# Kernel tuning notes

Measured on AMD Instinct MI355X. Metric: run time of the kernel, lower is better.

Reference implementation:

```python
import jax, jax.numpy as jnp
import numpy as np

B, S, D = 32, 1024, 1024
H = 16            # attention heads
T = 8             # num_tasks (probe tokens)
E = 8             # num_experts
K = 2             # top_k
HID = 4 * D       # expert hidden dim
EPS = 1e-5


def setup_inputs() -> dict:
    key = jax.random.key(0)
    ks = jax.random.split(key, 12)
    sd = 1.0 / np.sqrt(D)
    inp = {
        "x": jax.random.normal(ks[0], (B, S, D), jnp.float32),
        "probe": jax.random.normal(ks[1], (1, T, D), jnp.float32) * 0.02,
        "in_proj_w": jax.random.normal(ks[2], (3 * D, D), jnp.float32) * sd,
        "in_proj_b": jnp.zeros((3 * D,), jnp.float32),
        "out_proj_w": jax.random.normal(ks[3], (D, D), jnp.float32) * sd,
        "out_proj_b": jnp.zeros((D,), jnp.float32),
        "ln_gamma": jnp.ones((D,), jnp.float32),
        "ln_beta": jnp.zeros((D,), jnp.float32),
        "gate_w": jax.random.normal(ks[4], (T, D, E), jnp.float32) * sd,  # per-task gate (task-aware)
        "w1": jax.random.normal(ks[5], (E, D, HID), jnp.float32) * sd,
        "b1": jnp.zeros((E, HID), jnp.float32),
        "w2": jax.random.normal(ks[6], (E, HID, D), jnp.float32) / np.sqrt(HID),
        "b2": jnp.zeros((E, D), jnp.float32),
    }
    return inp


def reference(x, probe, in_proj_w, in_proj_b, out_proj_w, out_proj_b,
              ln_gamma, ln_beta, gate_w, w1, b1, w2, b2):
    b, s, d = x.shape
    t = probe.shape[1]
    dh = d // H
    # --- multihead cross attention: query = probe, key/value = x ---
    wq, wk, wv = in_proj_w[:d], in_proj_w[d:2 * d], in_proj_w[2 * d:]
    bq, bk, bv = in_proj_b[:d], in_proj_b[d:2 * d], in_proj_b[2 * d:]
    q = jnp.broadcast_to(probe, (b, t, d)) @ wq.T + bq           # [B,T,D]
    k = x @ wk.T + bk                                            # [B,S,D]
    v = x @ wv.T + bv
    q = q.reshape(b, t, H, dh).transpose(0, 2, 1, 3)             # bhtd
    k = k.reshape(b, s, H, dh).transpose(0, 2, 1, 3)             # bhsd
    v = v.reshape(b, s, H, dh).transpose(0, 2, 1, 3)
    scores = jnp.einsum('bhtd,bhsd->bhts', q, k) / np.sqrt(dh)
    attn = jax.nn.softmax(scores, axis=-1)                       # [B,H,T,S]
    ctx = jnp.einsum('bhts,bhsd->bhtd', attn, v)
    ctx = ctx.transpose(0, 2, 1, 3).reshape(b, t, d)
    attn_out = ctx @ out_proj_w.T + out_proj_b                   # [B,T,D]
    attn_weights = attn.mean(axis=1)                             # torch avg over heads
    # --- layernorm ---
    mu = attn_out.mean(-1, keepdims=True)
    var = attn_out.var(-1, keepdims=True)
    y = (attn_out - mu) * jax.lax.rsqrt(var + EPS) * ln_gamma + ln_beta
    # --- task-aware MoE: per-task gate, top-k routing ---
    logits = jnp.einsum('btd,tde->bte', y, gate_w)               # [B,T,E]
    probs = jax.nn.softmax(logits, axis=-1)
    tok = y.reshape(b * t, d)
    p = probs.reshape(b * t, E)
    topv, topi = jax.lax.top_k(p, K)                             # [N,K]
    wgt = topv / topv.sum(-1, keepdims=True)
    gates = jnp.zeros((b * t, E), y.dtype).at[jnp.arange(b * t)[:, None], topi].set(wgt)
    # all experts on all tokens (N=B*T is small); grouped GEMM form
    h = jax.nn.gelu(jnp.einsum('nd,edh->enh', tok, w1) + b1[:, None, :], approximate=False)
    eo = jnp.einsum('enh,ehd->end', h, w2) + b2[:, None, :]      # [E,N,D]
    moe_out = jnp.einsum('ne,end->nd', gates, eo).reshape(b, t, d)
    # load-balancing aux loss
    dispatch = (jax.nn.one_hot(topi, E, dtype=y.dtype)).sum(1)   # [N,E] 0/1
    f = dispatch.mean(0)
    P = p.mean(0)
    moe_loss = E * jnp.sum(f * P)
    final = attn_out + moe_out
    return final, moe_loss, attn_weights
```

## Files before the change

kernel.cpp:

```cpp
#include <hip/hip_runtime.h>
#include <hip/hip_bf16.h>
#include <math.h>


using bf16x8  = __attribute__((ext_vector_type(8))) short;
using f32x4   = __attribute__((ext_vector_type(4))) float;
using short4v = __attribute__((ext_vector_type(4))) short;

__device__ inline short f2bf(float f) {
  unsigned u = __builtin_bit_cast(unsigned, f);
  u = (u + 0x7fffu + ((u >> 16) & 1u)) >> 16;
  return (short)u;
}

static constexpr long OFF_Q       = 0;
static constexpr long OFF_QW      = 8192;
static constexpr long OFF_QB      = 139264;
static constexpr long OFF_PSUM    = 139392;
static constexpr long OFF_FCNT    = 139400;
static constexpr long OFF_GATES   = 139408;
static constexpr long OFF_CTX     = 141456;
static constexpr long OFF_ATTNOUT = 403600;
static constexpr long OFF_EO      = 665744;
static constexpr long OFF_CTXP    = 2762896;
static constexpr long OFF_AOP     = 3811472;
static constexpr long OFF_SCORES  = 4860048;
static constexpr long OFF_AX      = 13248656;
static constexpr long OFF_YB      = 21637264;
static constexpr long OFF_HB      = 21768336;

__global__ __launch_bounds__(256) void compute_q_k(const float* __restrict__ probe,
                                                   const float* __restrict__ in_w,
                                                   const float* __restrict__ in_b,
                                                   float* __restrict__ q) {
  int wid = threadIdx.x >> 6, lane = threadIdx.x & 63;
  int idx = blockIdx.x * 4 + wid;
  int t = idx >> 10, d = idx & 1023;
  const float* pr = probe + (long)t * 1024;
  const float* wr = in_w + (long)d * 1024;
  float s = 0.f;
  for (int k = lane * 4; k < 1024; k += 256) {
    float4 a = *(const float4*)&pr[k];
    float4 b = *(const float4*)&wr[k];
    s += a.x * b.x + a.y * b.y + a.z * b.z + a.w * b.w;
  }
  for (int o = 32; o; o >>= 1) s += __shfl_xor(s, o);
  if (!lane) q[idx] = s + in_b[d];
}

__global__ __launch_bounds__(256) void compute_qw_k(const float* __restrict__ q,
                                                    const float* __restrict__ in_w,
                                                    const float* __restrict__ in_b,
                                                    float* __restrict__ qw,
                                                    float* __restrict__ qb) {
  const int h = blockIdx.y;
  const int tid = threadIdx.x;
  const int d = blockIdx.x * 256 + tid;
  __shared__ float qh[8][64];
  if (tid < 64) {
#pragma unroll
    for (int t = 0; t < 8; ++t) qh[t][tid] = q[t * 1024 + h * 64 + tid] * 0.125f;
  }
  __syncthreads();
  const float* wk = in_w + 1048576 + (long)h * 64 * 1024;
  float acc[8];
#pragma unroll
  for (int t = 0; t < 8; ++t) acc[t] = 0.f;
  for (int j = 0; j < 64; ++j) {
    float w = wk[(long)j * 1024 + d];
#pragma unroll
    for (int t = 0; t < 8; ++t) acc[t] += qh[t][j] * w;
  }
#pragma unroll
  for (int t = 0; t < 8; ++t) qw[(long)(h * 8 + t) * 1024 + d] = acc[t];
  if (blockIdx.x == 0 && tid < 8) {
    float s = 0.f;
    for (int j = 0; j < 64; ++j) s += qh[tid][j] * in_b[1024 + h * 64 + j];
    qb[h * 8 + tid] = s;
  }
}

template<int WM, int WN, int KS, bool AKB, bool BTRANS, bool A2S, int EPI>
__global__ __launch_bounds__(WM * WN * 64)
void gemm_ss(const float* __restrict__ Ap, const float* __restrict__ Bp,
             const float* __restrict__ kbias, float* __restrict__ Cp,
             int lda, int ldb, int K,
             long zA, long zA2, long zB, long zC, long ZKC, int ldc) {
  constexpr int BM = WM * 64, BN = WN * 64, BK = 32, NT = WM * WN * 64, PK = 40;
  constexpr int LA = BM * BK / (NT * 4), LB = BN * BK / (NT * 4);
  constexpr int F4 = BN / 4;
  const int z = blockIdx.z, zo = z / KS, kc = z % KS;
  const float* A = Ap + zA * zo + (long)kc * K;
  const float* B = BTRANS ? (Bp + zB * zo + (long)kc * K * ldb)
                          : (Bp + zB * zo + (long)kc * K);
  const float* kb = kbias + (long)kc * K;
  float* C = Cp + zC * zo + ZKC * kc;
  const int tid = threadIdx.x;
  const int m0 = blockIdx.y * BM, n0 = blockIdx.x * BN;
  __shared__ short Ah[BM][PK], Al[BM][PK], Bh[BN][PK], Bl[BN][PK];

  f32x4 acc[4][4];
#pragma unroll
  for (int i = 0; i < 4; ++i)
#pragma unroll
    for (int j = 0; j < 4; ++j)
#pragma unroll
      for (int qq = 0; qq < 4; ++qq) acc[i][j][qq] = 0.f;

  const int wid = tid >> 6, lane = tid & 63;
  const int wm = wid % WM, wn = wid / WM;
  const int r = lane & 15, kg = (lane >> 4) * 8;

  float4 ra[LA], rb[LB];

  auto loadT = [&](int k0) {
#pragma unroll
    for (int i = 0; i < LA; ++i) {
      int f = tid + i * NT;
      int m = f >> 3, k4 = (f & 7) * 4;
      long ofs = (long)(m0 + m) * lda + k0 + k4;
      ra[i] = *(const float4*)&A[ofs];
      if (A2S) {
        float4 v2 = *(const float4*)&A[ofs + zA2];
        ra[i].x += v2.x; ra[i].y += v2.y; ra[i].z += v2.z; ra[i].w += v2.w;
      }
      if (AKB) {
        float4 kv = *(const float4*)&kb[k0 + k4];
        ra[i].x += kv.x; ra[i].y += kv.y; ra[i].z += kv.z; ra[i].w += kv.w;
      }
    }
#pragma unroll
    for (int i = 0; i < LB; ++i) {
      int f = tid + i * NT;
      if (BTRANS) {
        int k = f / F4, n4 = (f % F4) * 4;
        rb[i] = *(const float4*)&B[(long)(k0 + k) * ldb + n0 + n4];
      } else {
        int n = f >> 3, k4 = (f & 7) * 4;
        rb[i] = *(const float4*)&B[(long)(n0 + n) * ldb + k0 + k4];
      }
    }
  };

  auto storeT = [&]() {
#pragma unroll
    for (int i = 0; i < LA; ++i) {
      int f = tid + i * NT;
      int m = f >> 3, k4 = (f & 7) * 4;
      short4v h, l;
      float vv[4] = {ra[i].x, ra[i].y, ra[i].z, ra[i].w};
#pragma unroll
      for (int j = 0; j < 4; ++j) {
        unsigned u = __builtin_bit_cast(unsigned, vv[j]);
        h[j] = (short)(u >> 16);
        l[j] = f2bf(vv[j] - __builtin_bit_cast(float, u & 0xFFFF0000u));
      }
      *(short4v*)&Ah[m][k4] = h;
      *(short4v*)&Al[m][k4] = l;
    }
#pragma unroll
    for (int i = 0; i < LB; ++i) {
      int f = tid + i * NT;
      float vv[4] = {rb[i].x, rb[i].y, rb[i].z, rb[i].w};
      if (BTRANS) {
        int k = f / F4, n4 = (f % F4) * 4;
#pragma unroll
        for (int j = 0; j < 4; ++j) {
          unsigned u = __builtin_bit_cast(unsigned, vv[j]);
          Bh[n4 + j][k] = (short)(u >> 16);
          Bl[n4 + j][k] = f2bf(vv[j] - __builtin_bit_cast(float, u & 0xFFFF0000u));
        }
      } else {
        int n = f >> 3, k4 = (f & 7) * 4;
        short4v h, l;
#pragma unroll
        for (int j = 0; j < 4; ++j) {
          unsigned u = __builtin_bit_cast(unsigned, vv[j]);
          h[j] = (short)(u >> 16);
          l[j] = f2bf(vv[j] - __builtin_bit_cast(float, u & 0xFFFF0000u));
        }
        *(short4v*)&Bh[n][k4] = h;
        *(short4v*)&Bl[n][k4] = l;
      }
    }
  };

  loadT(0);
  for (int k0 = 0; k0 < K; k0 += BK) {
    storeT();
    __syncthreads();
    if (k0 + BK < K) loadT(k0 + BK);
    bf16x8 ah[4], al[4], bh[4], bl[4];
#pragma unroll
    for (int i = 0; i < 4; ++i) {
      ah[i] = *(const bf16x8*)&Ah[wm * 64 + i * 16 + r][kg];
      al[i] = *(const bf16x8*)&Al[wm * 64 + i * 16 + r][kg];
    }
#pragma unroll
    for (int j = 0; j < 4; ++j) {
      bh[j] = *(const bf16x8*)&Bh[wn * 64 + j * 16 + r][kg];
      bl[j] = *(const bf16x8*)&Bl[wn * 64 + j * 16 + r][kg];
    }
#pragma unroll
    for (int i = 0; i < 4; ++i)
#pragma unroll
      for (int j = 0; j < 4; ++j) {
        acc[i][j] = __builtin_amdgcn_mfma_f32_16x16x32_bf16(ah[i], bh[j], acc[i][j], 0, 0, 0);
        acc[i][j] = __builtin_amdgcn_mfma_f32_16x16x32_bf16(ah[i], bl[j], acc[i][j], 0, 0, 0);
        acc[i][j] = __builtin_amdgcn_mfma_f32_16x16x32_bf16(al[i], bh[j], acc[i][j], 0, 0, 0);
      }
    __syncthreads();
  }

  const int q4 = (lane >> 4) * 4;
#pragma unroll
  for (int i = 0; i < 4; ++i) {
    int gmb = m0 + wm * 64 + i * 16 + q4;
#pragma unroll
    for (int j = 0; j < 4; ++j) {
      int gn = n0 + wn * 64 + j * 16 + r;
      if constexpr (EPI == 1) {
        float4 v;
        v.x = acc[i][j][0]; v.y = acc[i][j][1]; v.z = acc[i][j][2]; v.w = acc[i][j][3];
        *(float4*)&C[(long)(gmb >> 10) * 131072 + (long)gn * 1024 + (gmb & 1023)] = v;
      } else {
#pragma unroll
        for (int qq = 0; qq < 4; ++qq) {
          float v = acc[i][j][qq];
          int m = gmb + qq;
          if constexpr (EPI == 0) {
            C[(long)m * ldc + gn] = v;
          } else {
            C[(long)(m >> 3) * 262144 + (long)(m & 7) * 1024 + gn] = v;
          }
        }
      }
    }
  }
}

template<int WM, int WN, int KS, int EPI>
__global__ __launch_bounds__(WM * WN * 64)
void gemm_moe(const short* __restrict__ Ap, const float* __restrict__ Bp,
              const float* __restrict__ biasp, void* __restrict__ Cp,
              int lda, int ldb, int K, long zA, long zB, long zBias, long zC, int ldc) {
  constexpr int BM = WM * 64, BN = WN * 64, BK = 32, NT = WM * WN * 64, PK = 40;
  constexpr int LA = BM * BK / (NT * 8), LB = BN * BK / (NT * 4);
  constexpr int F4 = BN / 4;
  const int z = blockIdx.z, zo = z / KS, kc = z % KS;
  const short* A = Ap + zA * zo + (long)kc * K;
  const float* B = Bp + zB * zo + (long)kc * K * ldb;
  const float* bias = biasp + zBias * zo;
  const int tid = threadIdx.x;
  const int m0 = blockIdx.y * BM, n0 = blockIdx.x * BN;
  __shared__ short As[BM][PK], Bs[BN][PK];

  f32x4 acc[4][4];
#pragma unroll
  for (int i = 0; i < 4; ++i)
#pragma unroll
    for (int j = 0; j < 4; ++j)
#pragma unroll
      for (int qq = 0; qq < 4; ++qq) acc[i][j][qq] = 0.f;

  const int wid = tid >> 6, lane = tid & 63;
  const int wm = wid % WM, wn = wid / WM;
  const int r = lane & 15, kg = (lane >> 4) * 8;

  bf16x8 ra[LA];
  float4 rb[LB];

  auto loadT = [&](int k0) {
#pragma unroll
    for (int i = 0; i < LA; ++i) {
      int f = tid + i * NT;
      int m = f >> 2, k8 = (f & 3) * 8;
      ra[i] = *(const bf16x8*)&A[(long)(m0 + m) * lda + k0 + k8];
    }
#pragma unroll
    for (int i = 0; i < LB; ++i) {
      int f = tid + i * NT;
      int k = f / F4, n4 = (f % F4) * 4;
      rb[i] = *(const float4*)&B[(long)(k0 + k) * ldb + n0 + n4];
    }
  };

  loadT(0);
  for (int k0 = 0; k0 < K; k0 += BK) {
#pragma unroll
    for (int i = 0; i < LA; ++i) {
      int f = tid + i * NT;
      int m = f >> 2, k8 = (f & 3) * 8;
      *(bf16x8*)&As[m][k8] = ra[i];
    }
#pragma unroll
    for (int i = 0; i < LB; ++i) {
      int f = tid + i * NT;
      int k = f / F4, n4 = (f % F4) * 4;
      Bs[n4 + 0][k] = f2bf(rb[i].x);
      Bs[n4 + 1][k] = f2bf(rb[i].y);
      Bs[n4 + 2][k] = f2bf(rb[i].z);
      Bs[n4 + 3][k] = f2bf(rb[i].w);
    }
    __syncthreads();
    if (k0 + BK < K) loadT(k0 + BK);
    bf16x8 af[4], bfr[4];
#pragma unroll
    for (int i = 0; i < 4; ++i) af[i] = *(const bf16x8*)&As[wm * 64 + i * 16 + r][kg];
#pragma unroll
    for (int j = 0; j < 4; ++j) bfr[j] = *(const bf16x8*)&Bs[wn * 64 + j * 16 + r][kg];
#pragma unroll
    for (int i = 0; i < 4; ++i)
#pragma unroll
      for (int j = 0; j < 4; ++j)
        acc[i][j] = __builtin_amdgcn_mfma_f32_16x16x32_bf16(af[i], bfr[j], acc[i][j], 0, 0, 0);
    __syncthreads();
  }

  const int q4 = (lane >> 4) * 4;
#pragma unroll
  for (int i = 0; i < 4; ++i) {
    int gmb = m0 + wm * 64 + i * 16 + q4;
#pragma unroll
    for (int j = 0; j < 4; ++j) {
      int gn = n0 + wn * 64 + j * 16 + r;
#pragma unroll
      for (int qq = 0; qq < 4; ++qq) {
        float v = acc[i][j][qq];
        int m = gmb + qq;
        if constexpr (EPI == 2) {
          float u = v + bias[gn];
          u = 0.5f * u * (1.0f + erff(u * 0.70710678118654752f));
          ((short*)Cp + zC * zo)[(long)m * ldc + gn] = f2bf(u);
        } else {
          atomicAdd(&((float*)Cp + zC * zo)[(long)m * ldc + gn], v);
        }
      }
    }
  }
}

__global__ __launch_bounds__(256) void reduce4_k(const float* __restrict__ p,
                                                 float* __restrict__ out) {
  int i = (blockIdx.x * 256 + threadIdx.x) * 4;
  float4 a = *(const float4*)&p[i];
  float4 b = *(const float4*)&p[i + 262144];
  float4 c = *(const float4*)&p[i + 524288];
  float4 d = *(const float4*)&p[i + 786432];
  float4 o;
  o.x = a.x + b.x + c.x + d.x;
  o.y = a.y + b.y + c.y + d.y;
  o.z = a.z + b.z + c.z + d.z;
  o.w = a.w + b.w + c.w + d.w;
  *(float4*)&out[i] = o;
}

__global__ __launch_bounds__(256) void softmax_k(float* __restrict__ scores,
                                                 const float* __restrict__ qb) {
  long row = blockIdx.x;
  int ht = (int)(row & 127);
  float bias = qb[ht];
  float* p = scores + row * 1024;
  const float* p2 = p + 4194304;
  int tid = threadIdx.x;
  int wid = tid >> 6, lane = tid & 63;
  float v[4];
  float mx = -1e30f;
#pragma unroll
  for (int i = 0; i < 4; ++i) {
    int idx = tid + i * 256;
    v[i] = p[idx] + p2[idx] + bias;
    mx = fmaxf(mx, v[i]);
  }
  for (int o = 32; o; o >>= 1) mx = fmaxf(mx, __shfl_xor(mx, o));
  __shared__ float sm[4];
  __shared__ float ss[4];
  if (!lane) sm[wid] = mx;
  __syncthreads();
  mx = fmaxf(fmaxf(sm[0], sm[1]), fmaxf(sm[2], sm[3]));
  float s = 0.f;
#pragma unroll
  for (int i = 0; i < 4; ++i) { v[i] = expf(v[i] - mx); s += v[i]; }
  for (int o = 32; o; o >>= 1) s += __shfl_xor(s, o);
  if (!lane) ss[wid] = s;
  __syncthreads();
  s = ss[0] + ss[1] + ss[2] + ss[3];
  float inv = 1.0f / s;
#pragma unroll
  for (int i = 0; i < 4; ++i) p[tid + i * 256] = v[i] * inv;
}

__global__ __launch_bounds__(256) void attnw_k(const float* __restrict__ attn,
                                               float* __restrict__ outw) {
  int idx = blockIdx.x * 256 + threadIdx.x;
  int b = idx >> 13;
  int r = idx & 8191;
  int t = r >> 10, s = r & 1023;
  const float* p = attn + (long)b * 131072 + (long)t * 1024 + s;
  float acc = 0.f;
#pragma unroll
  for (int h = 0; h < 16; ++h) acc += p[(long)h * 8192];
  outw[idx] = acc * (1.0f / 16.0f);
}

__global__ __launch_bounds__(256) void ln_gate_k(const float* __restrict__ aop,
                                                 const float* __restrict__ out_b,
                                                 const float* __restrict__ gamma,
                                                 const float* __restrict__ beta,
                                                 const float* __restrict__ gate_w,
                                                 float* __restrict__ attn_out,
                                                 short* __restrict__ yb,
                                                 float* __restrict__ gates,
                                                 float* __restrict__ Psum,
                                                 float* __restrict__ fcnt) {
  int row = blockIdx.x;
  int t = row & 7;
  int tid = threadIdx.x;
  int wid = tid >> 6, lane = tid & 63;
  const float* xr = aop + (long)row * 1024;
  float vals[4];
  float s = 0.f, sq = 0.f;
#pragma unroll
  for (int i = 0; i < 4; ++i) {
    int d = tid + i * 256;
    float v = xr[d] + xr[d + 262144] + xr[d + 524288] + xr[d + 786432] + out_b[d];
    attn_out[(long)row * 1024 + d] = v;
    vals[i] = v;
    s += v;
    sq += v * v;
  }
  for (int o = 32; o; o >>= 1) { s += __shfl_xor(s, o); sq += __shfl_xor(sq, o); }
  __shared__ float rs[4], rss[4];
  if (!lane) { rs[wid] = s; rss[wid] = sq; }
  __syncthreads();
  s = rs[0] + rs[1] + rs[2] + rs[3];
  sq = rss[0] + rss[1] + rss[2] + rss[3];
  float mu = s * (1.0f / 1024.0f);
  float var = sq * (1.0f / 1024.0f) - mu * mu;
  float rstd = rsqrtf(var + 1e-5f);
  __shared__ float yrow[1024];
#pragma unroll
  for (int i = 0; i < 4; ++i) {
    int d = tid + i * 256;
    float yv = (vals[i] - mu) * rstd * gamma[d] + beta[d];
    yb[(long)row * 1024 + d] = f2bf(yv);
    yrow[d] = yv;
  }
  __syncthreads();
  int e = tid & 7;
  int g = tid >> 3;
  float acc = 0.f;
  const float* gw = gate_w + (long)t * 8192;
  for (int d = g; d < 1024; d += 32) acc += yrow[d] * gw[d * 8 + e];
  __shared__ float part[256];
  __shared__ float lsh[8];
  part[tid] = acc;
  __syncthreads();
  if (tid < 8) {
    float l = 0.f;
    for (int gg = 0; gg < 32; ++gg) l += part[gg * 8 + tid];
    lsh[tid] = l;
  }
  __syncthreads();
  if (tid == 0) {
    float p[8];
    float mx = -1e30f;
    for (int k = 0; k < 8; ++k) mx = fmaxf(mx, lsh[k]);
    float sum = 0.f;
    for (int k = 0; k < 8; ++k) { p[k] = expf(lsh[k] - mx); sum += p[k]; }
    float inv = 1.0f / sum;
    for (int k = 0; k < 8; ++k) p[k] *= inv;
    int i0 = 0;
    for (int k = 1; k < 8; ++k) if (p[k] > p[i0]) i0 = k;
    int i1 = -1;
    for (int k = 0; k < 8; ++k) if (k != i0 && (i1 < 0 || p[k] > p[i1])) i1 = k;
    float tot = p[i0] + p[i1];
    for (int k = 0; k < 8; ++k)
      gates[(long)row * 8 + k] = (k == i0) ? p[i0] / tot : (k == i1) ? p[i1] / tot : 0.f;
    for (int k = 0; k < 8; ++k) atomicAdd(&Psum[k], p[k]);
    atomicAdd(&fcnt[i0], 1.0f);
    atomicAdd(&fcnt[i1], 1.0f);
  }
}

__global__ __launch_bounds__(256) void combine_k(const float* __restrict__ attn_out,
                                                 const float* __restrict__ eo,
                                                 const float* __restrict__ b2,
                                                 const float* __restrict__ gates,
                                                 float* __restrict__ outp) {
  int idx = blockIdx.x * 256 + threadIdx.x;
  int n = idx >> 10, d = idx & 1023;
  float v = attn_out[idx];
  const float* g = gates + (long)n * 8;
#pragma unroll
  for (int e = 0; e < 8; ++e) {
    float ge = g[e];
    if (ge != 0.f) v += ge * (eo[(long)e * 262144 + idx] + b2[e * 1024 + d]);
  }
  outp[idx] = v;
}

__global__ void loss_k(const float* __restrict__ Psum, const float* __restrict__ fcnt,
                       float* __restrict__ out) {
  if (threadIdx.x == 0) {
    float l = 0.f;
    for (int e = 0; e < 8; ++e) l += (fcnt[e] * (1.0f / 256.0f)) * (Psum[e] * (1.0f / 256.0f));
    out[0] = 8.0f * l;
  }
}

extern "C" void kernel_launch(void* const* d_in, const int* in_sizes, int n_in,
                              void* d_out, int out_size, void* d_ws, size_t ws_size,
                              hipStream_t stream) {
  const float* x      = (const float*)d_in[0];
  const float* probe  = (const float*)d_in[1];
  const float* in_w   = (const float*)d_in[2];
  const float* in_b   = (const float*)d_in[3];
  const float* out_w  = (const float*)d_in[4];
  const float* out_b  = (const float*)d_in[5];
  const float* gamma  = (const float*)d_in[6];
  const float* beta   = (const float*)d_in[7];
  const float* gate_w = (const float*)d_in[8];
  const float* w1     = (const float*)d_in[9];
  const float* b1     = (const float*)d_in[10];
  const float* w2     = (const float*)d_in[11];
  const float* b2     = (const float*)d_in[12];

  float* ws = (float*)d_ws;
  float* q        = ws + OFF_Q;
  float* qw       = ws + OFF_QW;
  float* qb       = ws + OFF_QB;
  float* Psum     = ws + OFF_PSUM;
  float* fcnt     = ws + OFF_FCNT;
  float* gates    = ws + OFF_GATES;
  float* ctx      = ws + OFF_CTX;
  float* attn_out = ws + OFF_ATTNOUT;
  float* eo       = ws + OFF_EO;
  float* ctxp     = ws + OFF_CTXP;
  float* aop      = ws + OFF_AOP;
  float* scores   = ws + OFF_SCORES;
  float* axp      = ws + OFF_AX;
  short* yb       = (short*)(ws + OFF_YB);
  short* hb       = (short*)(ws + OFF_HB);

  float* out_final = (float*)d_out;
  float* out_loss  = out_final + 262144;
  float* out_attnw = out_loss + 1;

  hipMemsetAsync(ws + OFF_PSUM, 0, 16 * sizeof(float), stream);
  hipMemsetAsync(eo, 0, 2097152 * sizeof(float), stream);

  compute_q_k<<<2048, 256, 0, stream>>>(probe, in_w, in_b, q);
  compute_qw_k<<<dim3(4, 16, 1), 256, 0, stream>>>(q, in_w, in_b, qw, qb);

  gemm_ss<2, 2, 2, false, false, false, 1><<<dim3(1, 256, 2), 256, 0, stream>>>(
      x, qw, qb , scores, 1024, 1024, 512,
      0L, 0L, 0L, 0L, 4194304L, 1024);

  softmax_k<<<4096, 256, 0, stream>>>(scores, qb);
  attnw_k<<<1024, 256, 0, stream>>>(scores, out_attnw);

  gemm_ss<2, 2, 2, false, true, false, 4><<<dim3(8, 1, 64), 256, 0, stream>>>(
      scores, x, qb , axp, 1024, 1024, 512,
      131072L, 0L, 1048576L, 8192L, 4194304L, 1024);

  gemm_ss<1, 1, 4, false, false, true, 0><<<dim3(1, 4, 64), 64, 0, stream>>>(
      axp, in_w + 2097152, qb , ctxp, 1024, 1024, 256,
      262144L, 4194304L, 65536L, 64L, 262144L, 1024);
  reduce4_k<<<256, 256, 0, stream>>>(ctxp, ctx);

  gemm_ss<1, 1, 4, true, false, false, 0><<<dim3(16, 4, 4), 64, 0, stream>>>(
      ctx, out_w, in_b + 2048, aop, 1024, 1024, 256,
      0L, 0L, 0L, 0L, 262144L, 1024);

  ln_gate_k<<<256, 256, 0, stream>>>(aop, out_b, gamma, beta, gate_w, attn_out,
                                     yb, gates, Psum, fcnt);

  gemm_moe<4, 2, 1, 2><<<dim3(32, 1, 8), 512, 0, stream>>>(
      yb, w1, b1, hb, 1024, 4096, 1024, 0L, 4194304L, 4096L, 1048576L, 4096);

  gemm_moe<4, 2, 4, 5><<<dim3(8, 1, 32), 512, 0, stream>>>(
      hb, w2, b1 , eo, 4096, 1024, 1024, 1048576L, 4194304L, 0L, 262144L, 1024);

  combine_k<<<1024, 256, 0, stream>>>(attn_out, eo, b2, gates, out_final);
  loss_k<<<1, 64, 0, stream>>>(Psum, fcnt, out_loss);
}
```

Baseline: 406.8 us.

## Use single-bf16 scores GEMM, deeper split-K, swizzled B tiles, smaller MoE blocks

Replaces the split-bf16 (hi/lo, three MFMA) scores GEMM with a plain bf16 GEMM that uses one MFMA per tile. It raises split-K from 2 to 4 for the scores and attention-x GEMMs, and the softmax and ctx GEMM now sum four partials. It also XOR-swizzles the transposed B tiles in shared memory to cut LDS bank conflicts, and switches the MoE GEMMs from 512-thread blocks to 256-thread blocks with twice the grid. The single-bf16 scores lose precision in the attention logits, and the extra split-K partials cost more workspace and more memory traffic.

```diff
diff --git a/kernel.cpp b/kernel.cpp
--- a/kernel.cpp
+++ b/kernel.cpp
@@ -11,6 +11,9 @@
   unsigned u = __builtin_bit_cast(unsigned, f);
   u = (u + 0x7fffu + ((u >> 16) & 1u)) >> 16;
   return (short)u;
+}
+__device__ inline int bswz(int k, int n) {
+  return (((k >> 3) ^ ((n >> 2) & 3)) << 3) | (k & 7);
 }
 
 static constexpr long OFF_Q       = 0;
@@ -25,9 +28,9 @@
 static constexpr long OFF_CTXP    = 2762896;
 static constexpr long OFF_AOP     = 3811472;
 static constexpr long OFF_SCORES  = 4860048;
-static constexpr long OFF_AX      = 13248656;
-static constexpr long OFF_YB      = 21637264;
-static constexpr long OFF_HB      = 21768336;
+static constexpr long OFF_AX      = 21637264;
+static constexpr long OFF_YB      = 38414480;
+static constexpr long OFF_HB      = 38545552;
 
 __global__ __launch_bounds__(256) void compute_q_k(const float* __restrict__ probe,
                                                    const float* __restrict__ in_w,
@@ -80,7 +83,96 @@
   }
 }
 
-template<int WM, int WN, int KS, bool AKB, bool BTRANS, bool A2S, int EPI>
+template<int WM, int WN>
+__global__ __launch_bounds__(WM * WN * 64)
+void gemm_fb(const float* __restrict__ Ap, const float* __restrict__ Bp,
+             float* __restrict__ Cp, int lda, int ldb, int K, long ZKC) {
+  constexpr int BM = WM * 64, BN = WN * 64, BK = 32, NT = WM * WN * 64, PK = 40;
+  constexpr int LA = BM * BK / (NT * 4), LB = BN * BK / (NT * 4);
+  const int kc = blockIdx.z;
+  const float* A = Ap + (long)kc * K;
+  const float* B = Bp + (long)kc * K;
+  float* C = Cp + ZKC * kc;
+  const int tid = threadIdx.x;
+  const int m0 = blockIdx.y * BM, n0 = blockIdx.x * BN;
+  __shared__ short As[BM][PK], Bs[BN][PK];
+
+  f32x4 acc[4][4];
+#pragma unroll
+  for (int i = 0; i < 4; ++i)
+#pragma unroll
+    for (int j = 0; j < 4; ++j)
+#pragma unroll
+      for (int qq = 0; qq < 4; ++qq) acc[i][j][qq] = 0.f;
+
+  const int wid = tid >> 6, lane = tid & 63;
+  const int wm = wid % WM, wn = wid / WM;
+  const int r = lane & 15, kg = (lane >> 4) * 8;
+
+  float4 ra[LA], rb[LB];
+
+  auto loadT = [&](int k0) {
+#pragma unroll
+    for (int i = 0; i < LA; ++i) {
+      int f = tid + i * NT;
+      int m = f >> 3, k4 = (f & 7) * 4;
+      ra[i] = *(const float4*)&A[(long)(m0 + m) * lda + k0 + k4];
+    }
+#pragma unroll
+    for (int i = 0; i < LB; ++i) {
+      int f = tid + i * NT;
+      int n = f >> 3, k4 = (f & 7) * 4;
+      rb[i] = *(const float4*)&B[(long)(n0 + n) * ldb + k0 + k4];
+    }
+  };
+
+  loadT(0);
+  for (int k0 = 0; k0 < K; k0 += BK) {
+#pragma unroll
+    for (int i = 0; i < LA; ++i) {
+      int f = tid + i * NT;
+      int m = f >> 3, k4 = (f & 7) * 4;
+      short4v s;
+      s.x = f2bf(ra[i].x); s.y = f2bf(ra[i].y); s.z = f2bf(ra[i].z); s.w = f2bf(ra[i].w);
+      *(short4v*)&As[m][k4] = s;
+    }
+#pragma unroll
+    for (int i = 0; i < LB; ++i) {
+      int f = tid + i * NT;
+      int n = f >> 3, k4 = (f & 7) * 4;
+      short4v s;
+      s.x = f2bf(rb[i].x); s.y = f2bf(rb[i].y); s.z = f2bf(rb[i].z); s.w = f2bf(rb[i].w);
+      *(short4v*)&Bs[n][k4] = s;
+    }
+    __syncthreads();
+    if (k0 + BK < K) loadT(k0 + BK);
+    bf16x8 af[4], bfr[4];
+#pragma unroll
+    for (int i = 0; i < 4; ++i) af[i] = *(const bf16x8*)&As[wm * 64 + i * 16 + r][kg];
+#pragma unroll
+    for (int j = 0; j < 4; ++j) bfr[j] = *(const bf16x8*)&Bs[wn * 64 + j * 16 + r][kg];
+#pragma unroll
+    for (int i = 0; i < 4; ++i)
+#pragma unroll
+      for (int j = 0; j < 4; ++j)
+        acc[i][j] = __builtin_amdgcn_mfma_f32_16x16x32_bf16(af[i], bfr[j], acc[i][j], 0, 0, 0);
+    __syncthreads();
+  }
+
+#pragma unroll
+  for (int i = 0; i < 4; ++i) {
+    int gmb = m0 + wm * 64 + i * 16 + (lane >> 4) * 4;
+#pragma unroll
+    for (int j = 0; j < 4; ++j) {
+      int gn = n0 + wn * 64 + j * 16 + r;
+      float4 v;
+      v.x = acc[i][j][0]; v.y = acc[i][j][1]; v.z = acc[i][j][2]; v.w = acc[i][j][3];
+      *(float4*)&C[(long)(gmb >> 10) * 131072 + (long)gn * 1024 + (gmb & 1023)] = v;
+    }
+  }
+}
+
+template<int WM, int WN, int KS, bool AKB, bool BTRANS, int APL, int EPI>
 __global__ __launch_bounds__(WM * WN * 64)
 void gemm_ss(const float* __restrict__ Ap, const float* __restrict__ Bp,
              const float* __restrict__ kbias, float* __restrict__ Cp,
@@ -120,8 +212,9 @@
       int m = f >> 3, k4 = (f & 7) * 4;
       long ofs = (long)(m0 + m) * lda + k0 + k4;
       ra[i] = *(const float4*)&A[ofs];
-      if (A2S) {
-        float4 v2 = *(const float4*)&A[ofs + zA2];
+#pragma unroll
+      for (int p = 1; p < APL; ++p) {
+        float4 v2 = *(const float4*)&A[ofs + zA2 * p];
         ra[i].x += v2.x; ra[i].y += v2.y; ra[i].z += v2.z; ra[i].w += v2.w;
       }
       if (AKB) {
@@ -164,11 +257,12 @@
       float vv[4] = {rb[i].x, rb[i].y, rb[i].z, rb[i].w};
       if (BTRANS) {
         int k = f / F4, n4 = (f % F4) * 4;
+        int col = bswz(k, n4);
 #pragma unroll
         for (int j = 0; j < 4; ++j) {
           unsigned u = __builtin_bit_cast(unsigned, vv[j]);
-          Bh[n4 + j][k] = (short)(u >> 16);
-          Bl[n4 + j][k] = f2bf(vv[j] - __builtin_bit_cast(float, u & 0xFFFF0000u));
+          Bh[n4 + j][col] = (short)(u >> 16);
+          Bl[n4 + j][col] = f2bf(vv[j] - __builtin_bit_cast(float, u & 0xFFFF0000u));
         }
       } else {
         int n = f >> 3, k4 = (f & 7) * 4;
@@ -198,8 +292,10 @@
     }
 #pragma unroll
     for (int j = 0; j < 4; ++j) {
-      bh[j] = *(const bf16x8*)&Bh[wn * 64 + j * 16 + r][kg];
-      bl[j] = *(const bf16x8*)&Bl[wn * 64 + j * 16 + r][kg];
+      int brow = wn * 64 + j * 16 + r;
+      int bcol = BTRANS ? bswz(kg, brow) : kg;
+      bh[j] = *(const bf16x8*)&Bh[brow][bcol];
+      bl[j] = *(const bf16x8*)&Bl[brow][bcol];
     }
 #pragma unroll
     for (int i = 0; i < 4; ++i)
@@ -219,20 +315,14 @@
 #pragma unroll
     for (int j = 0; j < 4; ++j) {
       int gn = n0 + wn * 64 + j * 16 + r;
-      if constexpr (EPI == 1) {
-        float4 v;
-        v.x = acc[i][j][0]; v.y = acc[i][j][1]; v.z = acc[i][j][2]; v.w = acc[i][j][3];
-        *(float4*)&C[(long)(gmb >> 10) * 131072 + (long)gn * 1024 + (gmb & 1023)] = v;
-      } else {
-#pragma unroll
-        for (int qq = 0; qq < 4; ++qq) {
-          float v = acc[i][j][qq];
-          int m = gmb + qq;
-          if constexpr (EPI == 0) {
-            C[(long)m * ldc + gn] = v;
-          } else {
-            C[(long)(m >> 3) * 262144 + (long)(m & 7) * 1024 + gn] = v;
-          }
+#pragma unroll
+      for (int qq = 0; qq < 4; ++qq) {
+        float v = acc[i][j][qq];
+        int m = gmb + qq;
+        if constexpr (EPI == 0) {
+          C[(long)m * ldc + gn] = v;
+        } else {
+          C[(long)(m >> 3) * 262144 + (long)(m & 7) * 1024 + gn] = v;
         }
       }
     }
@@ -241,9 +331,9 @@
 
 template<int WM, int WN, int KS, int EPI>
 __global__ __launch_bounds__(WM * WN * 64)
-void gemm_moe(const short* __restrict__ Ap, const float* __restrict__ Bp,
-              const float* __restrict__ biasp, void* __restrict__ Cp,
-              int lda, int ldb, int K, long zA, long zB, long zBias, long zC, int ldc) {
+void gemm_bw(const short* __restrict__ Ap, const float* __restrict__ Bp,
+             const float* __restrict__ biasp, void* __restrict__ Cp,
+             int lda, int ldb, int K, long zA, long zB, long zBias, long zC, int ldc) {
   constexpr int BM = WM * 64, BN = WN * 64, BK = 32, NT = WM * WN * 64, PK = 40;
   constexpr int LA = BM * BK / (NT * 8), LB = BN * BK / (NT * 4);
   constexpr int F4 = BN / 4;
@@ -297,10 +387,11 @@
     for (int i = 0; i < LB; ++i) {
       int f = tid + i * NT;
       int k = f / F4, n4 = (f % F4) * 4;
-      Bs[n4 + 0][k] = f2bf(rb[i].x);
-      Bs[n4 + 1][k] = f2bf(rb[i].y);
-      Bs[n4 + 2][k] = f2bf(rb[i].z);
-      Bs[n4 + 3][k] = f2bf(rb[i].w);
+      int col = bswz(k, n4);
+      Bs[n4 + 0][col] = f2bf(rb[i].x);
+      Bs[n4 + 1][col] = f2bf(rb[i].y);
+      Bs[n4 + 2][col] = f2bf(rb[i].z);
+      Bs[n4 + 3][col] = f2bf(rb[i].w);
     }
     __syncthreads();
     if (k0 + BK < K) loadT(k0 + BK);
@@ -308,7 +399,10 @@
 #pragma unroll
     for (int i = 0; i < 4; ++i) af[i] = *(const bf16x8*)&As[wm * 64 + i * 16 + r][kg];
 #pragma unroll
-    for (int j = 0; j < 4; ++j) bfr[j] = *(const bf16x8*)&Bs[wn * 64 + j * 16 + r][kg];
+    for (int j = 0; j < 4; ++j) {
+      int brow = wn * 64 + j * 16 + r;
+      bfr[j] = *(const bf16x8*)&Bs[brow][bswz(kg, brow)];
+    }
 #pragma unroll
     for (int i = 0; i < 4; ++i)
 #pragma unroll
@@ -361,7 +455,6 @@
   int ht = (int)(row & 127);
   float bias = qb[ht];
   float* p = scores + row * 1024;
-  const float* p2 = p + 4194304;
   int tid = threadIdx.x;
   int wid = tid >> 6, lane = tid & 63;
   float v[4];
@@ -369,7 +462,7 @@
 #pragma unroll
   for (int i = 0; i < 4; ++i) {
     int idx = tid + i * 256;
-    v[i] = p[idx] + p2[idx] + bias;
+    v[i] = p[idx] + p[idx + 4194304] + p[idx + 8388608] + p[idx + 12582912] + bias;
     mx = fmaxf(mx, v[i]);
   }
   for (int o = 32; o; o >>= 1) mx = fmaxf(mx, __shfl_xor(mx, o));
@@ -553,34 +646,33 @@
   compute_q_k<<<2048, 256, 0, stream>>>(probe, in_w, in_b, q);
   compute_qw_k<<<dim3(4, 16, 1), 256, 0, stream>>>(q, in_w, in_b, qw, qb);
 
-  gemm_ss<2, 2, 2, false, false, false, 1><<<dim3(1, 256, 2), 256, 0, stream>>>(
-      x, qw, qb , scores, 1024, 1024, 512,
-      0L, 0L, 0L, 0L, 4194304L, 1024);
+  gemm_fb<2, 2><<<dim3(1, 256, 4), 256, 0, stream>>>(
+      x, qw, scores, 1024, 1024, 256, 4194304L);
 
   softmax_k<<<4096, 256, 0, stream>>>(scores, qb);
   attnw_k<<<1024, 256, 0, stream>>>(scores, out_attnw);
 
-  gemm_ss<2, 2, 2, false, true, false, 4><<<dim3(8, 1, 64), 256, 0, stream>>>(
-      scores, x, qb , axp, 1024, 1024, 512,
+  gemm_ss<2, 2, 4, false, true, 1, 4><<<dim3(8, 1, 128), 256, 0, stream>>>(
+      scores, x, qb , axp, 1024, 1024, 256,
       131072L, 0L, 1048576L, 8192L, 4194304L, 1024);
 
-  gemm_ss<1, 1, 4, false, false, true, 0><<<dim3(1, 4, 64), 64, 0, stream>>>(
+  gemm_ss<1, 1, 4, false, false, 4, 0><<<dim3(1, 4, 64), 64, 0, stream>>>(
       axp, in_w + 2097152, qb , ctxp, 1024, 1024, 256,
       262144L, 4194304L, 65536L, 64L, 262144L, 1024);
   reduce4_k<<<256, 256, 0, stream>>>(ctxp, ctx);
 
-  gemm_ss<1, 1, 4, true, false, false, 0><<<dim3(16, 4, 4), 64, 0, stream>>>(
+  gemm_ss<1, 1, 4, true, false, 1, 0><<<dim3(16, 4, 4), 64, 0, stream>>>(
       ctx, out_w, in_b + 2048, aop, 1024, 1024, 256,
       0L, 0L, 0L, 0L, 262144L, 1024);
 
   ln_gate_k<<<256, 256, 0, stream>>>(aop, out_b, gamma, beta, gate_w, attn_out,
                                      yb, gates, Psum, fcnt);
 
-  gemm_moe<4, 2, 1, 2><<<dim3(32, 1, 8), 512, 0, stream>>>(
+  gemm_bw<2, 2, 1, 2><<<dim3(32, 2, 8), 256, 0, stream>>>(
       yb, w1, b1, hb, 1024, 4096, 1024, 0L, 4194304L, 4096L, 1048576L, 4096);
 
-  gemm_moe<4, 2, 4, 5><<<dim3(8, 1, 32), 512, 0, stream>>>(
-      hb, w2, b1 , eo, 4096, 1024, 1024, 1048576L, 4194304L, 0L, 262144L, 1024);
+  gemm_bw<2, 2, 4, 5><<<dim3(8, 2, 32), 256, 0, stream>>>(
+      hb, w2, b2 , eo, 4096, 1024, 1024, 1048576L, 4194304L, 0L, 262144L, 1024);
 
   combine_k<<<1024, 256, 0, stream>>>(attn_out, eo, b2, gates, out_final);
   loss_k<<<1, 64, 0, stream>>>(Psum, fcnt, out_loss);
```

After: 437.9 us. +7.7%, slower.
